# Kernel tuning notes

Measured on AMD Instinct MI355X. Metric: run time of the kernel, lower is better.

## Reference

```python
import jax, jax.numpy as jnp
import numpy as np

C = 128   # in_channels == global_graph_width (required by residual add)
W = 128
LN_EPS = 1e-5


def _mlp3(x, Ws, bs):
    # three stacked Linear layers (Dense dropout is identity in eval)
    for i in range(3):
        x = x @ Ws[i].T + bs[i]
    return x


def setup_inputs() -> dict:
    key = jax.random.key(0)
    ks = jax.random.split(key, 12)
    B, N, M = 16, 2048, 2048
    x1 = jax.random.normal(ks[0], (B, N, C), dtype=jnp.float32)
    x2 = jax.random.normal(ks[1], (B, M, C), dtype=jnp.float32)
    valid_mask = jax.random.randint(ks[2], (B, N, M), 0, 2) == 1
    s = 1.0 / np.sqrt(C)
    q_w = jax.random.normal(ks[3], (3, W, C), dtype=jnp.float32) * s
    q_b = jnp.zeros((3, W), dtype=jnp.float32)
    k_w = jax.random.normal(ks[4], (3, W, C), dtype=jnp.float32) * s
    k_b = jnp.zeros((3, W), dtype=jnp.float32)
    v_w = jax.random.normal(ks[5], (3, W, C), dtype=jnp.float32) * s
    v_b = jnp.zeros((3, W), dtype=jnp.float32)
    ln_g = jnp.ones((W,), dtype=jnp.float32)
    ln_b = jnp.zeros((W,), dtype=jnp.float32)
    return {"x1": x1, "x2": x2, "valid_mask": valid_mask,
            "q_w": q_w, "q_b": q_b, "k_w": k_w, "k_b": k_b,
            "v_w": v_w, "v_b": v_b, "ln_g": ln_g, "ln_b": ln_b}


def reference(x1, x2, valid_mask, q_w, q_b, k_w, k_b, v_w, v_b, ln_g, ln_b):
    query = _mlp3(x1, q_w, q_b)          # [B,N,W]
    key = _mlp3(x2, k_w, k_b)            # [B,M,W]
    value = _mlp3(x2, v_w, v_b)          # [B,M,W]
    scores = jnp.einsum('bnw,bmw->bnm', query, key) / jnp.sqrt(jnp.float32(W))
    # masked softmax: masked_fill(True -> -1e12), softmax, then zero masked cols
    scores = jnp.where(valid_mask, jnp.float32(-1e12), scores)
    attn = jax.nn.softmax(scores, axis=-1) * (1.0 - valid_mask.astype(scores.dtype))
    x = jnp.einsum('bnm,bmw->bnw', attn, value)  # [B,N,W]
    mu = jnp.mean(x, axis=-1, keepdims=True)
    var = jnp.var(x, axis=-1, keepdims=True)
    ln = (x - mu) / jnp.sqrt(var + LN_EPS) * ln_g + ln_b
    return ln + x1
```

## Files before the change

### kernel.cpp

```cpp
#include <hip/hip_runtime.h>
#include <hip/hip_bf16.h>
#include <hip/hip_fp16.h>

typedef __hip_bfloat16 bf16;
typedef __attribute__((ext_vector_type(8))) short short8;
typedef __attribute__((ext_vector_type(4))) float f32x4;

#define MFMA(a, b, c) __builtin_amdgcn_mfma_f32_16x16x32_bf16((a), (b), (c), 0, 0, 0)
#define SPLIT 2

__global__ void detect_mask(const unsigned int* __restrict__ m, int* __restrict__ flag)
{
    __shared__ int bad;
    if (threadIdx.x == 0) bad = 0;
    __syncthreads();
    unsigned int w = m[threadIdx.x];
    bool ok = (w == 0u) || (w == 1u) || (w == 0x3F800000u);
    if (!ok) atomicAdd(&bad, 1);
    __syncthreads();
    if (threadIdx.x == 0) *flag = (bad == 0) ? 0 : 1;
}

__global__ void compose_a(const float* __restrict__ qw, const float* __restrict__ qb,
                          const float* __restrict__ kw, const float* __restrict__ kb,
                          const float* __restrict__ vw, const float* __restrict__ vb,
                          float* __restrict__ T, float* __restrict__ bt)
{
    int h = blockIdx.x >> 7;
    int i = blockIdx.x & 127;
    int j = threadIdx.x;
    const float* W = (h == 0) ? qw : (h == 1) ? kw : vw;
    const float* bv = (h == 0) ? qb : (h == 1) ? kb : vb;
    const float* W1 = W;
    const float* W2 = W + 128 * 128;
    float acc = 0.f;
    for (int k = 0; k < 128; ++k) acc += W2[i * 128 + k] * W1[k * 128 + j];
    T[h * 16384 + i * 128 + j] = acc;
    if (j == 0) {
        float bacc = 0.f;
        for (int k = 0; k < 128; ++k) bacc += W2[i * 128 + k] * bv[k];
        bt[h * 128 + i] = bacc + bv[128 + i];
    }
}

__global__ void compose_b(const float* __restrict__ qw, const float* __restrict__ qb,
                          const float* __restrict__ kw, const float* __restrict__ kb,
                          const float* __restrict__ vw, const float* __restrict__ vb,
                          const float* __restrict__ T, const float* __restrict__ bt,
                          bf16* __restrict__ Weff, float* __restrict__ beff)
{
    int h = blockIdx.x >> 7;
    int i = blockIdx.x & 127;
    int j = threadIdx.x;
    const float* W = (h == 0) ? qw : (h == 1) ? kw : vw;
    const float* bv = (h == 0) ? qb : (h == 1) ? kb : vb;
    const float* W3 = W + 2 * 128 * 128;
    const float* Th = T + h * 16384;
    float acc = 0.f;
    for (int k = 0; k < 128; ++k) acc += W3[i * 128 + k] * Th[k * 128 + j];
    float scale = (h == 0) ? (1.4426950408889634f * rsqrtf(128.0f)) : 1.0f;
    Weff[h * 16384 + i * 128 + j] = __float2bfloat16(acc * scale);
    if (j == 0) {
        float bacc = 0.f;
        for (int k = 0; k < 128; ++k) bacc += W3[i * 128 + k] * bt[h * 128 + k];
        beff[h * 128 + i] = (bacc + bv[256 + i]) * scale;
    }
}

__global__ __launch_bounds__(256) void proj_rm(
    const float* __restrict__ X, const bf16* __restrict__ Wb,
    const float* __restrict__ bias, bf16* __restrict__ Y)
{
    __shared__ alignas(16) char sX[64 * 256];
    int tid = threadIdx.x;
    int lane = tid & 63, wave = tid >> 6;
    int l16 = lane & 15, lhi = lane >> 4;
    long long r0 = (long long)blockIdx.x * 64;
    {
        int row = tid >> 2, seg = tid & 3;
        const float4* src = reinterpret_cast<const float4*>(X + (r0 + row) * 128 + seg * 32);
        int swz = (row & 7) << 4;
        char* dst0 = &sX[0] + row * 256;
#pragma unroll
        for (int i = 0; i < 8; ++i) {
            float4 v = src[i];
            bf16* d = (bf16*)(dst0 + ((seg * 64 + i * 8) ^ swz));
            d[0] = __float2bfloat16(v.x); d[1] = __float2bfloat16(v.y);
            d[2] = __float2bfloat16(v.z); d[3] = __float2bfloat16(v.w);
        }
    }
    __syncthreads();
    int rloc = wave * 16 + l16;
    int swzr = (rloc & 7) << 4;
    short8 a[4];
#pragma unroll
    for (int c4 = 0; c4 < 4; ++c4)
        a[c4] = *(const short8*)(&sX[0] + ((rloc * 256 + lhi * 16 + c4 * 64) ^ swzr));
    f32x4 acc[8] = {};
#pragma unroll
    for (int n = 0; n < 8; ++n) {
        const bf16* wr = Wb + (n * 16 + l16) * 128 + lhi * 8;
#pragma unroll
        for (int c4 = 0; c4 < 4; ++c4)
            acc[n] = MFMA(a[c4], *(const short8*)(wr + c4 * 32), acc[n]);
    }
#pragma unroll
    for (int n = 0; n < 8; ++n) {
        float bia = bias[l16 + 16 * n];
#pragma unroll
        for (int r = 0; r < 4; ++r) {
            long long q = r0 + wave * 16 + lhi * 4 + r;
            Y[q * 128 + l16 + 16 * n] = __float2bfloat16(acc[n][r] + bia);
        }
    }
}

__global__ __launch_bounds__(256) void proj_kvf(
    const float* __restrict__ X2,
    const bf16* __restrict__ Wk, const float* __restrict__ bk,
    const bf16* __restrict__ Wv, const float* __restrict__ bv,
    bf16* __restrict__ Kf, bf16* __restrict__ Vf, int M)
{
    __shared__ alignas(16) char sX[64 * 256];
    __shared__ alignas(16) char rbuf[64 * 256];
    int tid = threadIdx.x;
    int lane = tid & 63, wave = tid >> 6;
    int l16 = lane & 15, lhi = lane >> 4;
    long long r0 = (long long)blockIdx.x * 64;
    int b = (int)(r0 / M);
    int m0 = (int)(r0 % M);
    {
        int row = tid >> 2, seg = tid & 3;
        const float4* src = reinterpret_cast<const float4*>(X2 + (r0 + row) * 128 + seg * 32);
        int swz = (row & 7) << 4;
        char* dst0 = &sX[0] + row * 256;
#pragma unroll
        for (int i = 0; i < 8; ++i) {
            float4 v = src[i];
            bf16* d = (bf16*)(dst0 + ((seg * 64 + i * 8) ^ swz));
            d[0] = __float2bfloat16(v.x); d[1] = __float2bfloat16(v.y);
            d[2] = __float2bfloat16(v.z); d[3] = __float2bfloat16(v.w);
        }
    }
    __syncthreads();

    {
        int rloc = wave * 16 + l16;
        int swzr = (rloc & 7) << 4;
        short8 a[4];
#pragma unroll
        for (int c4 = 0; c4 < 4; ++c4)
            a[c4] = *(const short8*)(&sX[0] + ((rloc * 256 + lhi * 16 + c4 * 64) ^ swzr));
        f32x4 acc[8] = {};
#pragma unroll
        for (int n = 0; n < 8; ++n) {
            const bf16* wr = Wk + (n * 16 + l16) * 128 + lhi * 8;
#pragma unroll
            for (int c4 = 0; c4 < 4; ++c4)
                acc[n] = MFMA(a[c4], *(const short8*)(wr + c4 * 32), acc[n]);
        }
#pragma unroll
        for (int n = 0; n < 8; ++n) {
            float bia = bk[l16 + 16 * n];
#pragma unroll
            for (int r = 0; r < 4; ++r) {
                int row = wave * 16 + lhi * 4 + r;
                *(bf16*)(&rbuf[0] + ((row * 256 + (l16 + 16 * n) * 2) ^ ((row & 7) << 4))) =
                    __float2bfloat16(acc[n][r] + bia);
            }
        }
    }
    __syncthreads();
#pragma unroll
    for (int c4 = 0; c4 < 4; ++c4) {
        int row = wave * 16 + l16;
        short8 v = *(const short8*)(&rbuf[0] +
            ((row * 256 + c4 * 64 + lhi * 16) ^ ((row & 7) << 4)));
        long long tile = (r0 >> 4) + wave;
        *(short8*)(Kf + (tile * 4 + c4) * 512 + lane * 8) = v;
    }

    int w0 = wave * 32;
    short8 a2[2][4];
#pragma unroll
    for (int wt = 0; wt < 2; ++wt) {
        const bf16* wr = Wv + (w0 + wt * 16 + l16) * 128 + lhi * 8;
#pragma unroll
        for (int c4 = 0; c4 < 4; ++c4) a2[wt][c4] = *(const short8*)(wr + c4 * 32);
    }
    f32x4 acc2[2][4] = {};
#pragma unroll
    for (int mtl = 0; mtl < 4; ++mtl) {
        int rloc = mtl * 16 + l16;
        int swzr = (rloc & 7) << 4;
#pragma unroll
        for (int c4 = 0; c4 < 4; ++c4) {
            short8 xb = *(const short8*)(&sX[0] + ((rloc * 256 + lhi * 16 + c4 * 64) ^ swzr));
            acc2[0][mtl] = MFMA(a2[0][c4], xb, acc2[0][mtl]);
            acc2[1][mtl] = MFMA(a2[1][c4], xb, acc2[1][mtl]);
        }
    }
    __syncthreads();
#pragma unroll
    for (int wt = 0; wt < 2; ++wt) {
#pragma unroll
        for (int r = 0; r < 4; ++r) {
            int w = w0 + wt * 16 + lhi * 4 + r;
            float bia = bv[w];
#pragma unroll
            for (int mtl = 0; mtl < 4; ++mtl) {
                int mloc = mtl * 16 + l16;
                *(bf16*)(&rbuf[0] + ((w * 128 + mloc * 2) ^ ((w & 7) << 4))) =
                    __float2bfloat16(acc2[wt][mtl][r] + bia);
            }
        }
    }
    __syncthreads();
#pragma unroll
    for (int q = 0; q < 4; ++q) {
        int fr = wave * 4 + q;
        int gloc = fr >> 3, n = fr & 7;
        int row = n * 16 + l16;
        short8 v = *(const short8*)(&rbuf[0] +
            ((row * 128 + gloc * 64 + lhi * 16) ^ ((row & 7) << 4)));
        long long g = (long long)b * (M >> 5) + (m0 >> 5) + gloc;
        *(short8*)(Vf + (g * 8 + n) * 512 + lane * 8) = v;
    }
}

__global__ __launch_bounds__(256, 4) void attn_split(
    const bf16* __restrict__ Q, const bf16* __restrict__ Kf, const bf16* __restrict__ Vf,
    const void* __restrict__ maskp, const int* __restrict__ flagp,
    __half* __restrict__ pacc, float* __restrict__ pml,
    int B, int N, int M)
{
    __shared__ alignas(16) char kbuf[2][8192];
    __shared__ alignas(16) char vbuf[2][8192];
    __shared__ alignas(16) unsigned char smask[4][512];
    int nq = N >> 6;
    int nwg = gridDim.x;
    int bid = blockIdx.x;
    int wg = ((nwg & 7) == 0) ? ((bid & 7) * (nwg >> 3) + (bid >> 3)) : bid;
    int qt = wg % nq;
    int s  = (wg / nq) % SPLIT;
    int b  = wg / (nq * SPLIT);
    int tid = threadIdx.x;
    int lane = tid & 63, wave = tid >> 6;
    int l16 = lane & 15, lhi = lane >> 4;
    int q0 = qt * 64 + wave * 16;
    int Mh = M / SPLIT;
    int mbase = s * Mh;
    long long R = (long long)B * N;
    int fl4 = (*flagp == 0);
    const int NT = Mh >> 5;

    const bf16* qptr = Q + ((long long)b * N + q0 + l16) * 128 + lhi * 8;
    short8 aq[4];
#pragma unroll
    for (int c4 = 0; c4 < 4; ++c4) aq[c4] = *(const short8*)(qptr + c4 * 32);

    long long ktile0 = ((long long)b * M + mbase) >> 4;
    long long gbase  = ((long long)b * M + mbase) >> 5;

    int srow = lane >> 2, soff = (lane & 3) * 8;
    long long mrowb = ((long long)b * N + q0 + srow) * (long long)M + mbase + soff;

    unsigned char* smw = &smask[wave][0];

    f32x4 acc[8] = {};
    float plsum = 0.f;

    auto mload = [&](int t) -> uint2 {
        uint2 r;
        if (fl4) {
            const int* mp = (const int*)maskp;
            const int4* pp = (const int4*)(mp + mrowb + (long long)t * 32);
            int4 a = pp[0], bb = pp[1];
            r.x = (a.x ? 1u : 0u) | ((a.y ? 1u : 0u) << 8) |
                  ((a.z ? 1u : 0u) << 16) | ((a.w ? 1u : 0u) << 24);
            r.y = (bb.x ? 1u : 0u) | ((bb.y ? 1u : 0u) << 8) |
                  ((bb.z ? 1u : 0u) << 16) | ((bb.w ? 1u : 0u) << 24);
        } else {
            r = *(const uint2*)((const unsigned char*)maskp + mrowb + (long long)t * 32);
        }
        return r;
    };

    {
        long long F = ktile0 * 4 + wave * 2;
        long long G = gbase * 8 + wave * 2;
        int4 k0 = *(const int4*)(Kf + F * 512 + lane * 8);
        int4 k1 = *(const int4*)(Kf + (F + 1) * 512 + lane * 8);
        int4 v0 = *(const int4*)(Vf + G * 512 + lane * 8);
        int4 v1 = *(const int4*)(Vf + (G + 1) * 512 + lane * 8);
        uint2 mreg = mload(0);
        *(int4*)(&kbuf[0][(wave * 2 + 0) * 1024 + lane * 16]) = k0;
        *(int4*)(&kbuf[0][(wave * 2 + 1) * 1024 + lane * 16]) = k1;
        *(int4*)(&vbuf[0][(wave * 2 + 0) * 1024 + lane * 16]) = v0;
        *(int4*)(&vbuf[0][(wave * 2 + 1) * 1024 + lane * 16]) = v1;
        *(uint2*)(smw + srow * 32 + soff) = mreg;
        __syncthreads();
    }

    for (int t = 0; t < NT; ++t) {
        int cur = t & 1;
        int4 ks0, ks1, vs0, vs1;
        uint2 mreg;
        bool nxt = (t + 1 < NT);
        if (nxt) {
            long long F = (ktile0 + 2LL * (t + 1)) * 4 + wave * 2;
            long long G = (gbase + (t + 1)) * 8 + wave * 2;
            ks0 = *(const int4*)(Kf + F * 512 + lane * 8);
            ks1 = *(const int4*)(Kf + (F + 1) * 512 + lane * 8);
            vs0 = *(const int4*)(Vf + G * 512 + lane * 8);
            vs1 = *(const int4*)(Vf + (G + 1) * 512 + lane * 8);
            mreg = mload(t + 1);
        }

        __builtin_amdgcn_s_setprio(1);
        f32x4 sv[2];
#pragma unroll
        for (int j = 0; j < 2; ++j) {
            f32x4 tt = {0.f, 0.f, 0.f, 0.f};
#pragma unroll
            for (int c4 = 0; c4 < 4; ++c4)
                tt = MFMA(*(const short8*)(&kbuf[cur][(j * 4 + c4) * 1024 + lane * 16]),
                          aq[c4], tt);
            sv[j] = tt;
        }
        __builtin_amdgcn_s_setprio(0);

        uint2 Bb[2];
#pragma unroll
        for (int j = 0; j < 2; ++j) {
            unsigned int mk = *(const unsigned int*)(smw + l16 * 32 + 16 * j + lhi * 4);
            float p0 = (mk & 0x000000ffu) ? 0.f : exp2f(sv[j][0]);
            float p1 = (mk & 0x0000ff00u) ? 0.f : exp2f(sv[j][1]);
            float p2 = (mk & 0x00ff0000u) ? 0.f : exp2f(sv[j][2]);
            float p3 = (mk & 0xff000000u) ? 0.f : exp2f(sv[j][3]);
            plsum += (p0 + p1) + (p2 + p3);
            unsigned int w0, w1;
            asm("v_cvt_pk_bf16_f32 %0, %1, %2" : "=v"(w0) : "v"(p0), "v"(p1));
            asm("v_cvt_pk_bf16_f32 %0, %1, %2" : "=v"(w1) : "v"(p2), "v"(p3));
            Bb[j].x = w0; Bb[j].y = w1;
        }

        uint2 X1 = (lhi < 2) ? Bb[1] : Bb[0];
        uint2 Qb;
        Qb.x = __shfl_xor((int)X1.x, 32);
        Qb.y = __shfl_xor((int)X1.y, 32);
        uint2 Pb = (lhi < 2) ? Bb[0] : Bb[1];
        uint2 X2 = (lhi == 1 || lhi == 2) ? Pb : Qb;
        uint2 Y2;
        Y2.x = __shfl_xor((int)X2.x, 16);
        Y2.y = __shfl_xor((int)X2.y, 16);
        uint2 s0 = (lhi == 0) ? Pb : (lhi == 1) ? Y2 : (lhi == 2) ? Qb : Y2;
        uint2 s1 = (lhi == 0) ? Y2 : (lhi == 1) ? Qb : (lhi == 2) ? Y2 : Pb;
        unsigned int paw[4] = {s0.x, s0.y, s1.x, s1.y};
        short8 pa = *(const short8*)paw;

        __builtin_amdgcn_s_setprio(1);
#pragma unroll
        for (int n = 0; n < 8; ++n)
            acc[n] = MFMA(pa, *(const short8*)(&vbuf[cur][n * 1024 + lane * 16]), acc[n]);
        __builtin_amdgcn_s_setprio(0);

        if (nxt) {
            int nx = cur ^ 1;
            *(int4*)(&kbuf[nx][(wave * 2 + 0) * 1024 + lane * 16]) = ks0;
            *(int4*)(&kbuf[nx][(wave * 2 + 1) * 1024 + lane * 16]) = ks1;
            *(int4*)(&vbuf[nx][(wave * 2 + 0) * 1024 + lane * 16]) = vs0;
            *(int4*)(&vbuf[nx][(wave * 2 + 1) * 1024 + lane * 16]) = vs1;
            *(uint2*)(smw + srow * 32 + soff) = mreg;
            __syncthreads();
        }
    }

    float lsum = plsum;
    lsum += __shfl_xor(lsum, 16);
    lsum += __shfl_xor(lsum, 32);
    float invq = (lsum > 0.f) ? 1.f / lsum : 0.f;
    float inv[4];
#pragma unroll
    for (int r = 0; r < 4; ++r) inv[r] = __shfl(invq, lhi * 4 + r);
    long long rowg[4];
#pragma unroll
    for (int r = 0; r < 4; ++r) rowg[r] = (long long)b * N + q0 + lhi * 4 + r;
#pragma unroll
    for (int n = 0; n < 8; ++n)
#pragma unroll
        for (int r = 0; r < 4; ++r)
            pacc[((long long)s * R + rowg[r]) * 128 + l16 + 16 * n] =
                __float2half(acc[n][r] * inv[r]);
    if (lhi == 0)
        pml[(long long)s * R + (long long)b * N + q0 + l16] = lsum;
}

__global__ __launch_bounds__(256) void combine(
    const __half* __restrict__ pacc, const float* __restrict__ pml,
    const float* __restrict__ lng, const float* __restrict__ lnb,
    const float* __restrict__ x1, float* __restrict__ out, long long R)
{
    int tid = threadIdx.x;
    int lane = tid & 63, wave = tid >> 6;
    long long row = (long long)blockIdx.x * 4 + wave;
    float l[SPLIT];
    float den = 0.f;
#pragma unroll
    for (int s = 0; s < SPLIT; ++s) {
        l[s] = pml[(long long)s * R + row];
        den += l[s];
    }
    float inv = (den > 0.f) ? 1.f / den : 0.f;
    int c0 = lane * 2;
    float xa = 0.f, xb = 0.f;
#pragma unroll
    for (int s = 0; s < SPLIT; ++s) {
        const __half* hp = pacc + ((long long)s * R + row) * 128 + c0;
        xa += l[s] * __half2float(hp[0]);
        xb += l[s] * __half2float(hp[1]);
    }
    xa *= inv; xb *= inv;
    float su = xa + xb;
#pragma unroll
    for (int o = 1; o < 64; o <<= 1) su += __shfl_xor(su, o);
    float mu = su * (1.f / 128.f);
    float da = xa - mu, db = xb - mu;
    float sq = da * da + db * db;
#pragma unroll
    for (int o = 1; o < 64; o <<= 1) sq += __shfl_xor(sq, o);
    float rstd = rsqrtf(sq * (1.f / 128.f) + 1e-5f);
    float2 xr = *(const float2*)(x1 + row * 128 + c0);
    float2 o2;
    o2.x = da * rstd * lng[c0] + lnb[c0] + xr.x;
    o2.y = db * rstd * lng[c0 + 1] + lnb[c0 + 1] + xr.y;
    *(float2*)(out + row * 128 + c0) = o2;
}

extern "C" void kernel_launch(void* const* d_in, const int* in_sizes, int n_in,
                              void* d_out, int out_size, void* d_ws, size_t ws_size,
                              hipStream_t stream)
{
    const float* x1 = (const float*)d_in[0];
    const float* x2 = (const float*)d_in[1];
    const void* mask = d_in[2];
    const float* qw = (const float*)d_in[3];
    const float* qb = (const float*)d_in[4];
    const float* kw = (const float*)d_in[5];
    const float* kb = (const float*)d_in[6];
    const float* vw = (const float*)d_in[7];
    const float* vb = (const float*)d_in[8];
    const float* lng = (const float*)d_in[9];
    const float* lnb = (const float*)d_in[10];

    long long a = (long long)in_sizes[0] / 128;
    long long c = (long long)in_sizes[1] / 128;
    long long mm = (long long)in_sizes[2];
    int B = (int)((a * c) / mm);
    int N = (int)(a / B);
    int M = (int)(c / B);
    long long R = a;

    char* p = (char*)d_ws;
    bf16* Q = (bf16*)p;    p += (size_t)a * 128 * sizeof(bf16);
    bf16* Kf = (bf16*)p;   p += (size_t)c * 128 * sizeof(bf16);
    bf16* Vf = (bf16*)p;   p += (size_t)c * 128 * sizeof(bf16);
    float* T = (float*)p;  p += 3 * 128 * 128 * sizeof(float);
    float* bt = (float*)p; p += 3 * 128 * sizeof(float);
    float* beff = (float*)p; p += 3 * 128 * sizeof(float);
    bf16* Weff = (bf16*)p; p += 3 * 128 * 128 * sizeof(bf16);
    int* flag = (int*)p;   p += 256;
    __half* pacc = (__half*)p; p += (size_t)SPLIT * R * 128 * sizeof(__half);
    float* pml = (float*)p;    p += (size_t)SPLIT * R * sizeof(float);

    detect_mask<<<1, 256, 0, stream>>>((const unsigned int*)mask, flag);
    compose_a<<<384, 128, 0, stream>>>(qw, qb, kw, kb, vw, vb, T, bt);
    compose_b<<<384, 128, 0, stream>>>(qw, qb, kw, kb, vw, vb, T, bt, Weff, beff);

    proj_rm<<<(int)(a / 64), 256, 0, stream>>>(x1, Weff, beff, Q);
    proj_kvf<<<(int)(c / 64), 256, 0, stream>>>(x2, Weff + 16384, beff + 128,
                                                Weff + 2 * 16384, beff + 256, Kf, Vf, M);

    int nblk = B * (N / 64) * SPLIT;
    attn_split<<<nblk, 256, 0, stream>>>(Q, Kf, Vf, mask, flag, pacc, pml, B, N, M);
    combine<<<(int)(R / 4), 256, 0, stream>>>(pacc, pml, lng, lnb, x1, (float*)d_out, R);
}
```

Before: 159.7 us.

## Process two query groups per wave in attention to reuse K/V tiles

Each workgroup now covers 128 query rows instead of 64: each wave handles two 16-row query groups that share the same K and V fragments loaded from LDS. This halves the number of K/V global loads and LDS fills per query row and doubles MFMA work per LDS read. In exchange it doubles accumulator registers, lowering the occupancy target to 2 waves per SIMD, and halves the grid size. Mask traffic per row is unchanged.

```diff
diff --git a/kernel.cpp b/kernel.cpp
--- a/kernel.cpp
+++ b/kernel.cpp
@@ -228,7 +228,7 @@
     }
 }
 
-__global__ __launch_bounds__(256, 4) void attn_split(
+__global__ __launch_bounds__(256, 2) void attn_split(
     const bf16* __restrict__ Q, const bf16* __restrict__ Kf, const bf16* __restrict__ Vf,
     const void* __restrict__ maskp, const int* __restrict__ flagp,
     __half* __restrict__ pacc, float* __restrict__ pml,
@@ -236,8 +236,8 @@
 {
     __shared__ alignas(16) char kbuf[2][8192];
     __shared__ alignas(16) char vbuf[2][8192];
-    __shared__ alignas(16) unsigned char smask[4][512];
-    int nq = N >> 6;
+    __shared__ alignas(16) unsigned char smask[4][2][512];
+    int nq = N >> 7;
     int nwg = gridDim.x;
     int bid = blockIdx.x;
     int wg = ((nwg & 7) == 0) ? ((bid & 7) * (nwg >> 3) + (bid >> 3)) : bid;
@@ -247,30 +247,32 @@
     int tid = threadIdx.x;
     int lane = tid & 63, wave = tid >> 6;
     int l16 = lane & 15, lhi = lane >> 4;
-    int q0 = qt * 64 + wave * 16;
+    int q0 = qt * 128 + wave * 16;
     int Mh = M / SPLIT;
     int mbase = s * Mh;
     long long R = (long long)B * N;
     int fl4 = (*flagp == 0);
     const int NT = Mh >> 5;
 
-    const bf16* qptr = Q + ((long long)b * N + q0 + l16) * 128 + lhi * 8;
-    short8 aq[4];
-#pragma unroll
-    for (int c4 = 0; c4 < 4; ++c4) aq[c4] = *(const short8*)(qptr + c4 * 32);
+    short8 aq[2][4];
+#pragma unroll
+    for (int g = 0; g < 2; ++g) {
+        const bf16* qptr = Q + ((long long)b * N + q0 + g * 64 + l16) * 128 + lhi * 8;
+#pragma unroll
+        for (int c4 = 0; c4 < 4; ++c4) aq[g][c4] = *(const short8*)(qptr + c4 * 32);
+    }
 
     long long ktile0 = ((long long)b * M + mbase) >> 4;
     long long gbase  = ((long long)b * M + mbase) >> 5;
 
     int srow = lane >> 2, soff = (lane & 3) * 8;
-    long long mrowb = ((long long)b * N + q0 + srow) * (long long)M + mbase + soff;
-
-    unsigned char* smw = &smask[wave][0];
-
-    f32x4 acc[8] = {};
-    float plsum = 0.f;
-
-    auto mload = [&](int t) -> uint2 {
+    long long mrowb0 = ((long long)b * N + q0 + srow) * (long long)M + mbase + soff;
+    long long mrowb1 = mrowb0 + 64LL * M;
+
+    f32x4 acc[2][8] = {};
+    float plsum[2] = {0.f, 0.f};
+
+    auto mload = [&](long long mrowb, int t) -> uint2 {
         uint2 r;
         if (fl4) {
             const int* mp = (const int*)maskp;
@@ -293,19 +295,21 @@
         int4 k1 = *(const int4*)(Kf + (F + 1) * 512 + lane * 8);
         int4 v0 = *(const int4*)(Vf + G * 512 + lane * 8);
         int4 v1 = *(const int4*)(Vf + (G + 1) * 512 + lane * 8);
-        uint2 mreg = mload(0);
+        uint2 m0 = mload(mrowb0, 0);
+        uint2 m1 = mload(mrowb1, 0);
         *(int4*)(&kbuf[0][(wave * 2 + 0) * 1024 + lane * 16]) = k0;
         *(int4*)(&kbuf[0][(wave * 2 + 1) * 1024 + lane * 16]) = k1;
         *(int4*)(&vbuf[0][(wave * 2 + 0) * 1024 + lane * 16]) = v0;
         *(int4*)(&vbuf[0][(wave * 2 + 1) * 1024 + lane * 16]) = v1;
-        *(uint2*)(smw + srow * 32 + soff) = mreg;
+        *(uint2*)(&smask[wave][0][srow * 32 + soff]) = m0;
+        *(uint2*)(&smask[wave][1][srow * 32 + soff]) = m1;
         __syncthreads();
     }
 
     for (int t = 0; t < NT; ++t) {
         int cur = t & 1;
         int4 ks0, ks1, vs0, vs1;
-        uint2 mreg;
+        uint2 mr0, mr1;
         bool nxt = (t + 1 < NT);
         if (nxt) {
             long long F = (ktile0 + 2LL * (t + 1)) * 4 + wave * 2;
@@ -314,55 +318,62 @@
             ks1 = *(const int4*)(Kf + (F + 1) * 512 + lane * 8);
             vs0 = *(const int4*)(Vf + G * 512 + lane * 8);
             vs1 = *(const int4*)(Vf + (G + 1) * 512 + lane * 8);
-            mreg = mload(t + 1);
+            mr0 = mload(mrowb0, t + 1);
+            mr1 = mload(mrowb1, t + 1);
         }
 
         __builtin_amdgcn_s_setprio(1);
-        f32x4 sv[2];
-#pragma unroll
-        for (int j = 0; j < 2; ++j) {
-            f32x4 tt = {0.f, 0.f, 0.f, 0.f};
-#pragma unroll
-            for (int c4 = 0; c4 < 4; ++c4)
-                tt = MFMA(*(const short8*)(&kbuf[cur][(j * 4 + c4) * 1024 + lane * 16]),
-                          aq[c4], tt);
-            sv[j] = tt;
-        }
+        f32x4 sv[2][2] = {};
+#pragma unroll
+        for (int j = 0; j < 2; ++j)
+#pragma unroll
+            for (int c4 = 0; c4 < 4; ++c4) {
+                short8 kf = *(const short8*)(&kbuf[cur][(j * 4 + c4) * 1024 + lane * 16]);
+                sv[0][j] = MFMA(kf, aq[0][c4], sv[0][j]);
+                sv[1][j] = MFMA(kf, aq[1][c4], sv[1][j]);
+            }
         __builtin_amdgcn_s_setprio(0);
 
-        uint2 Bb[2];
-#pragma unroll
-        for (int j = 0; j < 2; ++j) {
-            unsigned int mk = *(const unsigned int*)(smw + l16 * 32 + 16 * j + lhi * 4);
-            float p0 = (mk & 0x000000ffu) ? 0.f : exp2f(sv[j][0]);
-            float p1 = (mk & 0x0000ff00u) ? 0.f : exp2f(sv[j][1]);
-            float p2 = (mk & 0x00ff0000u) ? 0.f : exp2f(sv[j][2]);
-            float p3 = (mk & 0xff000000u) ? 0.f : exp2f(sv[j][3]);
-            plsum += (p0 + p1) + (p2 + p3);
-            unsigned int w0, w1;
-            asm("v_cvt_pk_bf16_f32 %0, %1, %2" : "=v"(w0) : "v"(p0), "v"(p1));
-            asm("v_cvt_pk_bf16_f32 %0, %1, %2" : "=v"(w1) : "v"(p2), "v"(p3));
-            Bb[j].x = w0; Bb[j].y = w1;
-        }
-
-        uint2 X1 = (lhi < 2) ? Bb[1] : Bb[0];
-        uint2 Qb;
-        Qb.x = __shfl_xor((int)X1.x, 32);
-        Qb.y = __shfl_xor((int)X1.y, 32);
-        uint2 Pb = (lhi < 2) ? Bb[0] : Bb[1];
-        uint2 X2 = (lhi == 1 || lhi == 2) ? Pb : Qb;
-        uint2 Y2;
-        Y2.x = __shfl_xor((int)X2.x, 16);
-        Y2.y = __shfl_xor((int)X2.y, 16);
-        uint2 s0 = (lhi == 0) ? Pb : (lhi == 1) ? Y2 : (lhi == 2) ? Qb : Y2;
-        uint2 s1 = (lhi == 0) ? Y2 : (lhi == 1) ? Qb : (lhi == 2) ? Y2 : Pb;
-        unsigned int paw[4] = {s0.x, s0.y, s1.x, s1.y};
-        short8 pa = *(const short8*)paw;
+        short8 pa[2];
+#pragma unroll
+        for (int g = 0; g < 2; ++g) {
+            uint2 Bb[2];
+#pragma unroll
+            for (int j = 0; j < 2; ++j) {
+                unsigned int mk = *(const unsigned int*)(
+                    &smask[wave][g][l16 * 32 + 16 * j + lhi * 4]);
+                float p0 = (mk & 0x000000ffu) ? 0.f : exp2f(sv[g][j][0]);
+                float p1 = (mk & 0x0000ff00u) ? 0.f : exp2f(sv[g][j][1]);
+                float p2 = (mk & 0x00ff0000u) ? 0.f : exp2f(sv[g][j][2]);
+                float p3 = (mk & 0xff000000u) ? 0.f : exp2f(sv[g][j][3]);
+                plsum[g] += (p0 + p1) + (p2 + p3);
+                unsigned int w0, w1;
+                asm("v_cvt_pk_bf16_f32 %0, %1, %2" : "=v"(w0) : "v"(p0), "v"(p1));
+                asm("v_cvt_pk_bf16_f32 %0, %1, %2" : "=v"(w1) : "v"(p2), "v"(p3));
+                Bb[j].x = w0; Bb[j].y = w1;
+            }
+            uint2 X1 = (lhi < 2) ? Bb[1] : Bb[0];
+            uint2 Qb;
+            Qb.x = __shfl_xor((int)X1.x, 32);
+            Qb.y = __shfl_xor((int)X1.y, 32);
+            uint2 Pb = (lhi < 2) ? Bb[0] : Bb[1];
+            uint2 X2 = (lhi == 1 || lhi == 2) ? Pb : Qb;
+            uint2 Y2;
+            Y2.x = __shfl_xor((int)X2.x, 16);
+            Y2.y = __shfl_xor((int)X2.y, 16);
+            uint2 s0 = (lhi == 0) ? Pb : (lhi == 1) ? Y2 : (lhi == 2) ? Qb : Y2;
+            uint2 s1 = (lhi == 0) ? Y2 : (lhi == 1) ? Qb : (lhi == 2) ? Y2 : Pb;
+            unsigned int paw[4] = {s0.x, s0.y, s1.x, s1.y};
+            pa[g] = *(const short8*)paw;
+        }
 
         __builtin_amdgcn_s_setprio(1);
 #pragma unroll
-        for (int n = 0; n < 8; ++n)
-            acc[n] = MFMA(pa, *(const short8*)(&vbuf[cur][n * 1024 + lane * 16]), acc[n]);
+        for (int n = 0; n < 8; ++n) {
+            short8 vf = *(const short8*)(&vbuf[cur][n * 1024 + lane * 16]);
+            acc[0][n] = MFMA(pa[0], vf, acc[0][n]);
+            acc[1][n] = MFMA(pa[1], vf, acc[1][n]);
+        }
         __builtin_amdgcn_s_setprio(0);
 
         if (nxt) {
@@ -371,29 +382,34 @@
             *(int4*)(&kbuf[nx][(wave * 2 + 1) * 1024 + lane * 16]) = ks1;
             *(int4*)(&vbuf[nx][(wave * 2 + 0) * 1024 + lane * 16]) = vs0;
             *(int4*)(&vbuf[nx][(wave * 2 + 1) * 1024 + lane * 16]) = vs1;
-            *(uint2*)(smw + srow * 32 + soff) = mreg;
+            *(uint2*)(&smask[wave][0][srow * 32 + soff]) = mr0;
+            *(uint2*)(&smask[wave][1][srow * 32 + soff]) = mr1;
             __syncthreads();
         }
     }
 
-    float lsum = plsum;
-    lsum += __shfl_xor(lsum, 16);
-    lsum += __shfl_xor(lsum, 32);
-    float invq = (lsum > 0.f) ? 1.f / lsum : 0.f;
-    float inv[4];
-#pragma unroll
-    for (int r = 0; r < 4; ++r) inv[r] = __shfl(invq, lhi * 4 + r);
-    long long rowg[4];
-#pragma unroll
-    for (int r = 0; r < 4; ++r) rowg[r] = (long long)b * N + q0 + lhi * 4 + r;
-#pragma unroll
-    for (int n = 0; n < 8; ++n)
+#pragma unroll
+    for (int g = 0; g < 2; ++g) {
+        float lsum = plsum[g];
+        lsum += __shfl_xor(lsum, 16);
+        lsum += __shfl_xor(lsum, 32);
+        float invq = (lsum > 0.f) ? 1.f / lsum : 0.f;
+        float inv[4];
+#pragma unroll
+        for (int r = 0; r < 4; ++r) inv[r] = __shfl(invq, lhi * 4 + r);
+        long long rowg[4];
 #pragma unroll
         for (int r = 0; r < 4; ++r)
-            pacc[((long long)s * R + rowg[r]) * 128 + l16 + 16 * n] =
-                __float2half(acc[n][r] * inv[r]);
-    if (lhi == 0)
-        pml[(long long)s * R + (long long)b * N + q0 + l16] = lsum;
+            rowg[r] = (long long)b * N + q0 + g * 64 + lhi * 4 + r;
+#pragma unroll
+        for (int n = 0; n < 8; ++n)
+#pragma unroll
+            for (int r = 0; r < 4; ++r)
+                pacc[((long long)s * R + rowg[r]) * 128 + l16 + 16 * n] =
+                    __float2half(acc[g][n][r] * inv[r]);
+        if (lhi == 0)
+            pml[(long long)s * R + (long long)b * N + q0 + g * 64 + l16] = lsum;
+    }
 }
 
 __global__ __launch_bounds__(256) void combine(
@@ -481,7 +497,7 @@
     proj_kvf<<<(int)(c / 64), 256, 0, stream>>>(x2, Weff + 16384, beff + 128,
                                                 Weff + 2 * 16384, beff + 256, Kf, Vf, M);
 
-    int nblk = B * (N / 64) * SPLIT;
+    int nblk = B * (N / 128) * SPLIT;
     attn_split<<<nblk, 256, 0, stream>>>(Q, Kf, Vf, mask, flag, pacc, pml, B, N, M);
     combine<<<(int)(R / 4), 256, 0, stream>>>(pacc, pml, lng, lnb, x1, (float*)d_out, R);
 }
```

Measured after the change: 183.8 us. 1.15x slower.

## Switch attention to 32x32x16 MFMA with 32-row query tiles per wave

Applied to the files above, without the earlier changes.

The attention kernel moves from 16x16x32 to 32x32x16 bf16 MFMA, and each wave now handles 32 query rows, so a workgroup covers 128 rows. Each K/V tile loaded into shared memory is therefore reused by twice as many queries, and the P-matrix shuffle logic is simpler. The K/V fragment layouts written by the projection kernel are rearranged to match the new MFMA operand layout. The cost is more accumulator registers per wave, which is why launch bounds drop to 2 blocks per SM, and half as many workgroups in the grid, which lowers occupancy.

```diff
diff --git a/kernel.cpp b/kernel.cpp
--- a/kernel.cpp
+++ b/kernel.cpp
@@ -5,8 +5,10 @@
 typedef __hip_bfloat16 bf16;
 typedef __attribute__((ext_vector_type(8))) short short8;
 typedef __attribute__((ext_vector_type(4))) float f32x4;
+typedef __attribute__((ext_vector_type(16))) float f32x16;
 
 #define MFMA(a, b, c) __builtin_amdgcn_mfma_f32_16x16x32_bf16((a), (b), (c), 0, 0, 0)
+#define MFMA32(a, b, c) __builtin_amdgcn_mfma_f32_32x32x16_bf16((a), (b), (c), 0, 0, 0)
 #define SPLIT 2
 
 __global__ void detect_mask(const unsigned int* __restrict__ m, int* __restrict__ flag)
@@ -126,6 +128,7 @@
     int tid = threadIdx.x;
     int lane = tid & 63, wave = tid >> 6;
     int l16 = lane & 15, lhi = lane >> 4;
+    int l31 = lane & 31, lh5 = lane >> 5;
     long long r0 = (long long)blockIdx.x * 64;
     int b = (int)(r0 / M);
     int m0 = (int)(r0 % M);
@@ -171,13 +174,18 @@
         }
     }
     __syncthreads();
-#pragma unroll
-    for (int c4 = 0; c4 < 4; ++c4) {
-        int row = wave * 16 + l16;
-        short8 v = *(const short8*)(&rbuf[0] +
-            ((row * 256 + c4 * 64 + lhi * 16) ^ ((row & 7) << 4)));
-        long long tile = (r0 >> 4) + wave;
-        *(short8*)(Kf + (tile * 4 + c4) * 512 + lane * 8) = v;
+    {
+        int t32 = wave >> 1;
+        int fb = (wave & 1) * 4;
+#pragma unroll
+        for (int fi = 0; fi < 4; ++fi) {
+            int f = fb + fi;
+            int row = t32 * 32 + l31;
+            int colb = f * 32 + lh5 * 16;
+            short8 v = *(const short8*)(&rbuf[0] + row * 256 + (colb ^ ((row & 7) << 4)));
+            long long t32g = (r0 >> 5) + t32;
+            *(short8*)(Kf + (t32g * 8 + f) * 512 + lane * 8) = v;
+        }
     }
 
     int w0 = wave * 32;
@@ -216,19 +224,20 @@
         }
     }
     __syncthreads();
-#pragma unroll
-    for (int q = 0; q < 4; ++q) {
-        int fr = wave * 4 + q;
-        int gloc = fr >> 3, n = fr & 7;
-        int row = n * 16 + l16;
-        short8 v = *(const short8*)(&rbuf[0] +
-            ((row * 128 + gloc * 64 + lhi * 16) ^ ((row & 7) << 4)));
-        long long g = (long long)b * (M >> 5) + (m0 >> 5) + gloc;
-        *(short8*)(Vf + (g * 8 + n) * 512 + lane * 8) = v;
-    }
-}
-
-__global__ __launch_bounds__(256, 4) void attn_split(
+    {
+        int t32 = wave >> 1, kvh = wave & 1;
+#pragma unroll
+        for (int wc = 0; wc < 4; ++wc) {
+            int row = wc * 32 + l31;
+            int colb = t32 * 64 + kvh * 32 + lh5 * 16;
+            short8 v = *(const short8*)(&rbuf[0] + row * 128 + (colb ^ ((row & 7) << 4)));
+            long long g32 = (long long)b * (M >> 5) + (m0 >> 5) + t32;
+            *(short8*)(Vf + (g32 * 8 + kvh * 4 + wc) * 512 + lane * 8) = v;
+        }
+    }
+}
+
+__global__ __launch_bounds__(256, 2) void attn_split(
     const bf16* __restrict__ Q, const bf16* __restrict__ Kf, const bf16* __restrict__ Vf,
     const void* __restrict__ maskp, const int* __restrict__ flagp,
     __half* __restrict__ pacc, float* __restrict__ pml,
@@ -236,8 +245,8 @@
 {
     __shared__ alignas(16) char kbuf[2][8192];
     __shared__ alignas(16) char vbuf[2][8192];
-    __shared__ alignas(16) unsigned char smask[4][512];
-    int nq = N >> 6;
+    __shared__ alignas(16) unsigned char smask[4][1024];
+    int nq = N >> 7;
     int nwg = gridDim.x;
     int bid = blockIdx.x;
     int wg = ((nwg & 7) == 0) ? ((bid & 7) * (nwg >> 3) + (bid >> 3)) : bid;
@@ -246,123 +255,120 @@
     int b  = wg / (nq * SPLIT);
     int tid = threadIdx.x;
     int lane = tid & 63, wave = tid >> 6;
-    int l16 = lane & 15, lhi = lane >> 4;
-    int q0 = qt * 64 + wave * 16;
+    int l31 = lane & 31, hi = lane >> 5;
+    int q0w = qt * 128 + wave * 32;
     int Mh = M / SPLIT;
     int mbase = s * Mh;
     long long R = (long long)B * N;
     int fl4 = (*flagp == 0);
     const int NT = Mh >> 5;
 
-    const bf16* qptr = Q + ((long long)b * N + q0 + l16) * 128 + lhi * 8;
-    short8 aq[4];
-#pragma unroll
-    for (int c4 = 0; c4 < 4; ++c4) aq[c4] = *(const short8*)(qptr + c4 * 32);
-
-    long long ktile0 = ((long long)b * M + mbase) >> 4;
-    long long gbase  = ((long long)b * M + mbase) >> 5;
-
-    int srow = lane >> 2, soff = (lane & 3) * 8;
-    long long mrowb = ((long long)b * N + q0 + srow) * (long long)M + mbase + soff;
+    const bf16* qbase = Q + ((long long)b * N + q0w + l31) * 128 + hi * 8;
+    short8 aq[8];
+#pragma unroll
+    for (int f = 0; f < 8; ++f) aq[f] = *(const short8*)(qbase + f * 16);
+
+    long long kt32 = ((long long)b * M + mbase) >> 5;
+
+    int srow = lane >> 1, scol = (lane & 1) * 16;
+    long long mrowE = ((long long)b * N + q0w + srow) * (long long)M + mbase + scol;
 
     unsigned char* smw = &smask[wave][0];
 
-    f32x4 acc[8] = {};
+    f32x16 acc[4] = {};
     float plsum = 0.f;
 
-    auto mload = [&](int t) -> uint2 {
-        uint2 r;
-        if (fl4) {
-            const int* mp = (const int*)maskp;
-            const int4* pp = (const int4*)(mp + mrowb + (long long)t * 32);
-            int4 a = pp[0], bb = pp[1];
-            r.x = (a.x ? 1u : 0u) | ((a.y ? 1u : 0u) << 8) |
-                  ((a.z ? 1u : 0u) << 16) | ((a.w ? 1u : 0u) << 24);
-            r.y = (bb.x ? 1u : 0u) | ((bb.y ? 1u : 0u) << 8) |
-                  ((bb.z ? 1u : 0u) << 16) | ((bb.w ? 1u : 0u) << 24);
-        } else {
-            r = *(const uint2*)((const unsigned char*)maskp + mrowb + (long long)t * 32);
-        }
+    auto mloadB = [&](int t) -> int4 {
+        return *(const int4*)((const unsigned char*)maskp + mrowE + (long long)t * 32);
+    };
+    auto mload4 = [&](int t) -> int4 {
+        const int* mp = (const int*)maskp;
+        int4 r;
+        unsigned int wd[4];
+#pragma unroll
+        for (int c = 0; c < 4; ++c) {
+            int4 x = *(const int4*)(mp + mrowE + (long long)t * 32 + c * 4);
+            wd[c] = (x.x ? 1u : 0u) | ((x.y ? 1u : 0u) << 8) |
+                    ((x.z ? 1u : 0u) << 16) | ((x.w ? 1u : 0u) << 24);
+        }
+        r.x = (int)wd[0]; r.y = (int)wd[1]; r.z = (int)wd[2]; r.w = (int)wd[3];
         return r;
     };
 
     {
-        long long F = ktile0 * 4 + wave * 2;
-        long long G = gbase * 8 + wave * 2;
-        int4 k0 = *(const int4*)(Kf + F * 512 + lane * 8);
-        int4 k1 = *(const int4*)(Kf + (F + 1) * 512 + lane * 8);
-        int4 v0 = *(const int4*)(Vf + G * 512 + lane * 8);
-        int4 v1 = *(const int4*)(Vf + (G + 1) * 512 + lane * 8);
-        uint2 mreg = mload(0);
+        int4 k0 = *(const int4*)(Kf + (kt32 * 8 + wave * 2 + 0) * 512 + lane * 8);
+        int4 k1 = *(const int4*)(Kf + (kt32 * 8 + wave * 2 + 1) * 512 + lane * 8);
+        int4 v0 = *(const int4*)(Vf + (kt32 * 8 + wave * 2 + 0) * 512 + lane * 8);
+        int4 v1 = *(const int4*)(Vf + (kt32 * 8 + wave * 2 + 1) * 512 + lane * 8);
+        int4 mreg = fl4 ? mload4(0) : mloadB(0);
         *(int4*)(&kbuf[0][(wave * 2 + 0) * 1024 + lane * 16]) = k0;
         *(int4*)(&kbuf[0][(wave * 2 + 1) * 1024 + lane * 16]) = k1;
         *(int4*)(&vbuf[0][(wave * 2 + 0) * 1024 + lane * 16]) = v0;
         *(int4*)(&vbuf[0][(wave * 2 + 1) * 1024 + lane * 16]) = v1;
-        *(uint2*)(smw + srow * 32 + soff) = mreg;
+        *(int4*)(smw + srow * 32 + scol) = mreg;
         __syncthreads();
     }
 
     for (int t = 0; t < NT; ++t) {
         int cur = t & 1;
-        int4 ks0, ks1, vs0, vs1;
-        uint2 mreg;
+        int4 ks0, ks1, vs0, vs1, mreg;
         bool nxt = (t + 1 < NT);
         if (nxt) {
-            long long F = (ktile0 + 2LL * (t + 1)) * 4 + wave * 2;
-            long long G = (gbase + (t + 1)) * 8 + wave * 2;
+            long long F = (kt32 + t + 1) * 8 + wave * 2;
             ks0 = *(const int4*)(Kf + F * 512 + lane * 8);
             ks1 = *(const int4*)(Kf + (F + 1) * 512 + lane * 8);
-            vs0 = *(const int4*)(Vf + G * 512 + lane * 8);
-            vs1 = *(const int4*)(Vf + (G + 1) * 512 + lane * 8);
-            mreg = mload(t + 1);
+            vs0 = *(const int4*)(Vf + F * 512 + lane * 8);
+            vs1 = *(const int4*)(Vf + (F + 1) * 512 + lane * 8);
+            mreg = fl4 ? mload4(t + 1) : mloadB(t + 1);
         }
 
         __builtin_amdgcn_s_setprio(1);
-        f32x4 sv[2];
-#pragma unroll
-        for (int j = 0; j < 2; ++j) {
-            f32x4 tt = {0.f, 0.f, 0.f, 0.f};
-#pragma unroll
-            for (int c4 = 0; c4 < 4; ++c4)
-                tt = MFMA(*(const short8*)(&kbuf[cur][(j * 4 + c4) * 1024 + lane * 16]),
-                          aq[c4], tt);
-            sv[j] = tt;
-        }
+        f32x16 sv = {};
+#pragma unroll
+        for (int f = 0; f < 8; ++f)
+            sv = MFMA32(*(const short8*)(&kbuf[cur][f * 1024 + lane * 16]), aq[f], sv);
         __builtin_amdgcn_s_setprio(0);
 
-        uint2 Bb[2];
-#pragma unroll
-        for (int j = 0; j < 2; ++j) {
-            unsigned int mk = *(const unsigned int*)(smw + l16 * 32 + 16 * j + lhi * 4);
-            float p0 = (mk & 0x000000ffu) ? 0.f : exp2f(sv[j][0]);
-            float p1 = (mk & 0x0000ff00u) ? 0.f : exp2f(sv[j][1]);
-            float p2 = (mk & 0x00ff0000u) ? 0.f : exp2f(sv[j][2]);
-            float p3 = (mk & 0xff000000u) ? 0.f : exp2f(sv[j][3]);
+        uint2 Bb[4];
+#pragma unroll
+        for (int G = 0; G < 4; ++G) {
+            unsigned int mk = *(const unsigned int*)(smw + l31 * 32 + G * 8 + hi * 4);
+            float p0 = (mk & 0x000000ffu) ? 0.f : exp2f(sv[G * 4 + 0]);
+            float p1 = (mk & 0x0000ff00u) ? 0.f : exp2f(sv[G * 4 + 1]);
+            float p2 = (mk & 0x00ff0000u) ? 0.f : exp2f(sv[G * 4 + 2]);
+            float p3 = (mk & 0xff000000u) ? 0.f : exp2f(sv[G * 4 + 3]);
             plsum += (p0 + p1) + (p2 + p3);
             unsigned int w0, w1;
             asm("v_cvt_pk_bf16_f32 %0, %1, %2" : "=v"(w0) : "v"(p0), "v"(p1));
             asm("v_cvt_pk_bf16_f32 %0, %1, %2" : "=v"(w1) : "v"(p2), "v"(p3));
-            Bb[j].x = w0; Bb[j].y = w1;
-        }
-
-        uint2 X1 = (lhi < 2) ? Bb[1] : Bb[0];
-        uint2 Qb;
-        Qb.x = __shfl_xor((int)X1.x, 32);
-        Qb.y = __shfl_xor((int)X1.y, 32);
-        uint2 Pb = (lhi < 2) ? Bb[0] : Bb[1];
-        uint2 X2 = (lhi == 1 || lhi == 2) ? Pb : Qb;
-        uint2 Y2;
-        Y2.x = __shfl_xor((int)X2.x, 16);
-        Y2.y = __shfl_xor((int)X2.y, 16);
-        uint2 s0 = (lhi == 0) ? Pb : (lhi == 1) ? Y2 : (lhi == 2) ? Qb : Y2;
-        uint2 s1 = (lhi == 0) ? Y2 : (lhi == 1) ? Qb : (lhi == 2) ? Y2 : Pb;
-        unsigned int paw[4] = {s0.x, s0.y, s1.x, s1.y};
-        short8 pa = *(const short8*)paw;
+            Bb[G].x = w0; Bb[G].y = w1;
+        }
+
+        uint2 sA = hi ? Bb[0] : Bb[1];
+        uint2 rA;
+        rA.x = __shfl_xor((int)sA.x, 32);
+        rA.y = __shfl_xor((int)sA.y, 32);
+        uint2 sB = hi ? Bb[2] : Bb[3];
+        uint2 rB;
+        rB.x = __shfl_xor((int)sB.x, 32);
+        rB.y = __shfl_xor((int)sB.y, 32);
+        unsigned int paw0[4], paw1[4];
+        if (hi == 0) {
+            paw0[0] = Bb[0].x; paw0[1] = Bb[0].y; paw0[2] = rA.x; paw0[3] = rA.y;
+            paw1[0] = Bb[2].x; paw1[1] = Bb[2].y; paw1[2] = rB.x; paw1[3] = rB.y;
+        } else {
+            paw0[0] = rA.x; paw0[1] = rA.y; paw0[2] = Bb[1].x; paw0[3] = Bb[1].y;
+            paw1[0] = rB.x; paw1[1] = rB.y; paw1[2] = Bb[3].x; paw1[3] = Bb[3].y;
+        }
+        short8 pa0 = *(const short8*)paw0;
+        short8 pa1 = *(const short8*)paw1;
 
         __builtin_amdgcn_s_setprio(1);
 #pragma unroll
-        for (int n = 0; n < 8; ++n)
-            acc[n] = MFMA(pa, *(const short8*)(&vbuf[cur][n * 1024 + lane * 16]), acc[n]);
+        for (int wc = 0; wc < 4; ++wc) {
+            acc[wc] = MFMA32(pa0, *(const short8*)(&vbuf[cur][(0 * 4 + wc) * 1024 + lane * 16]), acc[wc]);
+            acc[wc] = MFMA32(pa1, *(const short8*)(&vbuf[cur][(1 * 4 + wc) * 1024 + lane * 16]), acc[wc]);
+        }
         __builtin_amdgcn_s_setprio(0);
 
         if (nxt) {
@@ -371,29 +377,30 @@
             *(int4*)(&kbuf[nx][(wave * 2 + 1) * 1024 + lane * 16]) = ks1;
             *(int4*)(&vbuf[nx][(wave * 2 + 0) * 1024 + lane * 16]) = vs0;
             *(int4*)(&vbuf[nx][(wave * 2 + 1) * 1024 + lane * 16]) = vs1;
-            *(uint2*)(smw + srow * 32 + soff) = mreg;
+            *(int4*)(smw + srow * 32 + scol) = mreg;
             __syncthreads();
         }
     }
 
-    float lsum = plsum;
-    lsum += __shfl_xor(lsum, 16);
-    lsum += __shfl_xor(lsum, 32);
+    float lsum = plsum + __shfl_xor(plsum, 32);
     float invq = (lsum > 0.f) ? 1.f / lsum : 0.f;
-    float inv[4];
-#pragma unroll
-    for (int r = 0; r < 4; ++r) inv[r] = __shfl(invq, lhi * 4 + r);
-    long long rowg[4];
-#pragma unroll
-    for (int r = 0; r < 4; ++r) rowg[r] = (long long)b * N + q0 + lhi * 4 + r;
-#pragma unroll
-    for (int n = 0; n < 8; ++n)
-#pragma unroll
-        for (int r = 0; r < 4; ++r)
-            pacc[((long long)s * R + rowg[r]) * 128 + l16 + 16 * n] =
-                __float2half(acc[n][r] * inv[r]);
-    if (lhi == 0)
-        pml[(long long)s * R + (long long)b * N + q0 + l16] = lsum;
+    float iv[16];
+#pragma unroll
+    for (int reg = 0; reg < 16; ++reg) {
+        int qr = (reg & 3) + 8 * (reg >> 2) + 4 * hi;
+        iv[reg] = __shfl(invq, qr);
+    }
+    long long brow = (long long)b * N + q0w;
+#pragma unroll
+    for (int wc = 0; wc < 4; ++wc)
+#pragma unroll
+        for (int reg = 0; reg < 16; ++reg) {
+            int qr = (reg & 3) + 8 * (reg >> 2) + 4 * hi;
+            pacc[((long long)s * R + brow + qr) * 128 + wc * 32 + l31] =
+                __float2half(acc[wc][reg] * iv[reg]);
+        }
+    if (lane < 32)
+        pml[(long long)s * R + brow + lane] = lsum;
 }
 
 __global__ __launch_bounds__(256) void combine(
@@ -481,7 +488,7 @@
     proj_kvf<<<(int)(c / 64), 256, 0, stream>>>(x2, Weff + 16384, beff + 128,
                                                 Weff + 2 * 16384, beff + 256, Kf, Vf, M);
 
-    int nblk = B * (N / 64) * SPLIT;
+    int nblk = B * (N / 128) * SPLIT;
     attn_split<<<nblk, 256, 0, stream>>>(Q, Kf, Vf, mask, flag, pacc, pml, B, N, M);
     combine<<<(int)(R / 4), 256, 0, stream>>>(pacc, pml, lng, lnb, x1, (float*)d_out, R);
 }
```

New measurement: 160.2 us. Within noise of the previous version (+0.3%).
